# Kernel tuning notes

Measured on AMD Instinct MI355X. Metric: run time of the kernel, lower is better.

The kernel has to match this reference:

```python
import jax, jax.numpy as jnp
import numpy as np

B, S, D, H, FFN = 4, 1024, 1024, 16, 4096
DH = D // H
EPS = 1e-5
NEG = -1e20


def _layer_norm(t, g, b):
    m = jnp.mean(t, axis=-1, keepdims=True)
    v = jnp.mean((t - m) ** 2, axis=-1, keepdims=True)
    return (t - m) / jnp.sqrt(v + EPS) * g + b


def setup_inputs() -> dict:
    key = jax.random.key(0)
    ks = jax.random.split(key, 16)
    std_attn = np.sqrt(2.0 / (D + D)).astype(np.float32)  # xavier normal
    lim1 = np.sqrt(6.0 / (D + FFN)).astype(np.float32)    # xavier uniform
    inp = {
        'tensor': jax.random.normal(ks[0], (B, S, D), jnp.float32),
        'mask': jnp.ones((B, S), jnp.int32),
        'wq': jax.random.normal(ks[1], (D, D), jnp.float32) * std_attn,
        'bq': jnp.zeros((D,), jnp.float32),
        'wk': jax.random.normal(ks[2], (D, D), jnp.float32) * std_attn,
        'bk': jnp.zeros((D,), jnp.float32),
        'wv': jax.random.normal(ks[3], (D, D), jnp.float32) * std_attn,
        'bv': jnp.zeros((D,), jnp.float32),
        'wo': jax.random.normal(ks[4], (D, D), jnp.float32) * std_attn,
        'bo': jnp.zeros((D,), jnp.float32),
        'ln1_g': jnp.ones((D,), jnp.float32),
        'ln1_b': jnp.zeros((D,), jnp.float32),
        'w1': jax.random.uniform(ks[5], (FFN, D), jnp.float32, -lim1, lim1),
        'b1': jnp.zeros((FFN,), jnp.float32),
        'w2': jax.random.uniform(ks[6], (D, FFN), jnp.float32, -lim1, lim1),
        'b2': jnp.zeros((D,), jnp.float32),
        'ln2_g': jnp.ones((D,), jnp.float32),
        'ln2_b': jnp.zeros((D,), jnp.float32),
    }
    return inp


def reference(tensor, mask, wq, bq, wk, bk, wv, bv, wo, bo,
              ln1_g, ln1_b, w1, b1, w2, b2, ln2_g, ln2_b):
    x = tensor
    scale = jnp.sqrt(jnp.float32(DH))
    # QKV projections -> [B, S, H, DH]
    q = (x @ wq.T + bq).reshape(B, S, H, DH)
    k = (x @ wk.T + bk).reshape(B, S, H, DH)
    v = (x @ wv.T + bv).reshape(B, S, H, DH)
    # scores [B, H, Sq, Sk]
    scores = jnp.einsum('bqhd,bkhd->bhqk', q / scale, k)
    blocked = (mask == 0)[:, None, None, :]  # True -> block
    scores = jnp.where(blocked, NEG, scores)
    attn = jax.nn.softmax(scores.astype(jnp.float32), axis=-1).astype(x.dtype)
    ctx = jnp.einsum('bhqk,bkhd->bqhd', attn, v).reshape(B, S, D)
    attn_out = ctx @ wo.T + bo
    # post-LN (variant='aiayn')
    t = _layer_norm(x + attn_out, ln1_g, ln1_b)
    ffn = jax.nn.relu(t @ w1.T + b1) @ w2.T + b2
    t = _layer_norm(t + ffn, ln2_g, ln2_b)
    t = t * mask[:, :, None].astype(t.dtype)
    return t
```

## Files before the change

### kernel.cpp

```cpp
#include <hip/hip_runtime.h>

typedef __bf16 bf16x8 __attribute__((ext_vector_type(8)));
typedef __bf16 bf16x4 __attribute__((ext_vector_type(4)));
typedef float f32x4 __attribute__((ext_vector_type(4)));
typedef float f32x16 __attribute__((ext_vector_type(16)));

#define BB 4
#define SS 1024
#define DD 1024
#define HH 16
#define DHH 64
#define FFN 4096

__device__ __forceinline__ void gload_lds16(const void* g, void* lds) {
  __builtin_amdgcn_global_load_lds(
      (const __attribute__((address_space(1))) unsigned int*)g,
      (__attribute__((address_space(3))) unsigned int*)lds, 16, 0, 0);
}

__global__ __launch_bounds__(256) void cvt_all_kernel(
    const float* __restrict__ x, const float* __restrict__ wq, const float* __restrict__ wk,
    const float* __restrict__ wv, const float* __restrict__ wo, const float* __restrict__ w1,
    const float* __restrict__ w2, __bf16* __restrict__ xb, __bf16* __restrict__ wqkvb,
    __bf16* __restrict__ wob, __bf16* __restrict__ w1b, __bf16* __restrict__ w2b)
{
  int i = blockIdx.x * 256 + threadIdx.x;
  const float* src; __bf16* dst; int off;
  if (i < 524288)       { src = x;  dst = xb;              off = i; }
  else if (i < 655360)  { src = wq; dst = wqkvb;           off = i - 524288; }
  else if (i < 786432)  { src = wk; dst = wqkvb + 1048576; off = i - 655360; }
  else if (i < 917504)  { src = wv; dst = wqkvb + 2097152; off = i - 786432; }
  else if (i < 1048576) { src = wo; dst = wob;             off = i - 917504; }
  else if (i < 1572864) { src = w1; dst = w1b;             off = i - 1048576; }
  else                  { src = w2; dst = w2b;             off = i - 1572864; }
  float4 a = *(const float4*)(src + off * 8);
  float4 b = *(const float4*)(src + off * 8 + 4);
  bf16x8 v;
  v[0] = (__bf16)a.x; v[1] = (__bf16)a.y; v[2] = (__bf16)a.z; v[3] = (__bf16)a.w;
  v[4] = (__bf16)b.x; v[5] = (__bf16)b.y; v[6] = (__bf16)b.z; v[7] = (__bf16)b.w;
  *(bf16x8*)(dst + off * 8) = v;
}

template<int MODE>
__global__ __launch_bounds__(512, 2) void gemm_8ph(
    const __bf16* __restrict__ Ag, const __bf16* __restrict__ Bg,
    const float* __restrict__ bias, void* __restrict__ outp,
    int M, int N, int K)
{
  __shared__ __bf16 LdsEl[65536];
  char* L = (char*)LdsEl;
  const int tid = threadIdx.x, wid = tid >> 6, lane = tid & 63;
  const int wm = wid >> 2, wn = wid & 3, bh = wn >> 1;
  const int lr = lane & 15, lg = lane >> 4;
  const int l8 = lane >> 3, l7 = lane & 7;

  const int gx = gridDim.x, nwg = gx * gridDim.y;
  const int wg = blockIdx.y * gx + blockIdx.x;
  const int swz = (wg & 7) * (nwg >> 3) + (wg >> 3);
  const int bm = (swz / gx) * 256, bn = (swz % gx) * 256;

  const int rowA0 = wn * 32;
  const int rowB0 = (wn & 1) * 64 + wm * 32;
  const size_t gAr = (size_t)(bm + wm * 128 + rowA0);
  const size_t gBr = (size_t)(bn + bh * 128 + rowB0);

  const __bf16* srcA[4]; const __bf16* srcB[4];
#pragma unroll
  for (int c = 0; c < 4; ++c) {
    int rwA = rowA0 + c * 8 + l8;
    int scA = (l7 * 16) ^ (((rwA >> 2) & 1) << 5);
    srcA[c] = Ag + (gAr + c * 8 + l8) * K + (scA >> 1);
    int rwB = rowB0 + c * 8 + l8;
    int scB = (l7 * 16) ^ (((rwB >> 2) & 1) << 5);
    srcB[c] = Bg + (gBr + c * 8 + l8) * K + (scB >> 1);
  }
  char* dA = L + wm * 16384 + rowA0 * 128;
  char* dB = L + 65536 + bh * 16384 + rowB0 * 128;

#define STGA4(TAU, KT) do { const int kt_ = (KT) * 64; \
    gload_lds16(srcA[0] + kt_, dA + (TAU) * 32768);          \
    gload_lds16(srcA[1] + kt_, dA + (TAU) * 32768 + 1024);   \
    gload_lds16(srcA[2] + kt_, dA + (TAU) * 32768 + 2048);   \
    gload_lds16(srcA[3] + kt_, dA + (TAU) * 32768 + 3072); } while (0)
#define STGB4(TAU, KT) do { const int kt_ = (KT) * 64; \
    gload_lds16(srcB[0] + kt_, dB + (TAU) * 32768);          \
    gload_lds16(srcB[1] + kt_, dB + (TAU) * 32768 + 1024);   \
    gload_lds16(srcB[2] + kt_, dB + (TAU) * 32768 + 2048);   \
    gload_lds16(srcB[3] + kt_, dB + (TAU) * 32768 + 3072); } while (0)

  f32x4 acc[8][4] = {};

  STGA4(0, 0); STGB4(0, 0); STGA4(1, 1); STGB4(1, 1);
  asm volatile("s_waitcnt vmcnt(0)" ::: "memory");
  __builtin_amdgcn_s_barrier();

#define PHASE(TAU, KS, IH, STGCODE, WAITCODE) do { \
    bf16x8 af[4]; \
    _Pragma("unroll") for (int i = 0; i < 4; ++i) { \
      int row = (IH) * 64 + i * 16 + lr; \
      int cb = ((KS) * 64 + lg * 16) ^ (((row >> 2) & 1) << 5); \
      af[i] = *(const bf16x8*)(L + ((TAU) * 2 + wm) * 16384 + row * 128 + cb); } \
    if ((IH) == 0) { \
      _Pragma("unroll") for (int j = 0; j < 4; ++j) { \
        int row = (wn & 1) * 64 + j * 16 + lr; \
        int cb = ((KS) * 64 + lg * 16) ^ (((row >> 2) & 1) << 5); \
        bfr[j] = *(const bf16x8*)(L + 65536 + ((TAU) * 2 + bh) * 16384 + row * 128 + cb); } } \
    STGCODE; \
    __builtin_amdgcn_s_barrier(); \
    __builtin_amdgcn_s_setprio(1); \
    _Pragma("unroll") for (int i = 0; i < 4; ++i) \
    _Pragma("unroll") for (int j = 0; j < 4; ++j) \
      acc[(IH) * 4 + i][j] = __builtin_amdgcn_mfma_f32_16x16x32_bf16(af[i], bfr[j], acc[(IH) * 4 + i][j], 0, 0, 0); \
    __builtin_amdgcn_s_setprio(0); \
    WAITCODE; \
    __builtin_amdgcn_s_barrier(); \
  } while (0)

  const int NT = K >> 7;
#pragma unroll 1
  for (int t = 0; t < NT; ++t) {
    const bool s1 = (t > 0);
    const bool s0 = (t + 1 < NT);
    bf16x8 bfr[4];
    PHASE(0, 0, 0, { if (s1) STGA4(1, 2 * t + 1); }, {});
    PHASE(0, 0, 1, { if (s1) STGB4(1, 2 * t + 1); }, {});
    PHASE(0, 1, 0, {}, {});
    PHASE(0, 1, 1, {}, { asm volatile("s_waitcnt vmcnt(0)" ::: "memory"); });
    PHASE(1, 0, 0, { if (s0) STGA4(0, 2 * t + 2); }, {});
    PHASE(1, 0, 1, { if (s0) STGB4(0, 2 * t + 2); }, {});
    PHASE(1, 1, 0, {}, {});
    PHASE(1, 1, 1, {}, { asm volatile("s_waitcnt vmcnt(0)" ::: "memory"); });
  }
#undef PHASE
#undef STGA4
#undef STGB4

#pragma unroll
  for (int ih = 0; ih < 2; ++ih)
#pragma unroll
    for (int i = 0; i < 4; ++i)
#pragma unroll
      for (int j = 0; j < 4; ++j)
#pragma unroll
        for (int r = 0; r < 4; ++r) {
          int row = bm + wm * 128 + ih * 64 + i * 16 + lg * 4 + r;
          int col = bn + wn * 64 + j * 16 + lr;
          float v = acc[ih * 4 + i][j][r];
          if constexpr (MODE == 3) {
            float t2 = v + bias[col];
            ((__bf16*)outp)[(size_t)row * N + col] = (__bf16)fmaxf(t2, 0.f);
          }
        }
}

template<int MODE>
__global__ __launch_bounds__(256, 2) void gemm_bt(
    const __bf16* __restrict__ A, const __bf16* __restrict__ Bw,
    const float* __restrict__ bias, const float* __restrict__ bias1, const float* __restrict__ bias2,
    const float* __restrict__ res, void* __restrict__ outp, void* __restrict__ out1,
    int M, int N, int K, int kLen, float scale)
{
  __shared__ __bf16 As[2][128 * 32];
  __shared__ __bf16 Bs[2][128 * 32];
  const int tid = threadIdx.x;
  const int wid = tid >> 6;
  const int lane = tid & 63;
  const int lr = lane & 15;
  const int lg = lane >> 4;

  const int gx = gridDim.x;
  const int nwg = gx * gridDim.y;
  const int wg = blockIdx.y * gx + blockIdx.x;
  const int swz = (wg & 7) * (nwg >> 3) + (wg >> 3);
  const int bm = (swz / gx) * 128;
  const int bn = (swz % gx) * 128;

  const int wm = (wid >> 1) * 64;
  const int wn = (wid & 1) * 64;

  int kBeg = 0, nk = K >> 5;
  if constexpr (MODE == 5) { kBeg = blockIdx.z * kLen; nk = kLen >> 5; }

  const int off = tid * 16;
  const int srow = off >> 6;
  const int scol = (off & 63) >> 1;
  const __bf16* gA0 = A + (size_t)(bm + srow) * K + kBeg + scol;
  const __bf16* gA1 = A + (size_t)(bm + 64 + srow) * K + kBeg + scol;
  const __bf16* gB0 = Bw + (size_t)(bn + srow) * K + kBeg + scol;
  const __bf16* gB1 = Bw + (size_t)(bn + 64 + srow) * K + kBeg + scol;
  char* lA = (char*)&As[0][0] + wid * 1024;
  char* lB = (char*)&Bs[0][0] + wid * 1024;

  f32x4 acc[4][4] = {};

#define STAGE(buf, kk) do { \
    gload_lds16(gA0 + (kk), lA + (buf) * 8192); \
    gload_lds16(gA1 + (kk), lA + (buf) * 8192 + 4096); \
    gload_lds16(gB0 + (kk), lB + (buf) * 8192); \
    gload_lds16(gB1 + (kk), lB + (buf) * 8192 + 4096); \
  } while (0)

  STAGE(0, 0);
  __syncthreads();
  for (int t = 0; t < nk; ++t) {
    const int cur = t & 1;
    if (t + 1 < nk) STAGE(cur ^ 1, (t + 1) << 5);
    bf16x8 af[4], bv[4];
#pragma unroll
    for (int i = 0; i < 4; ++i)
      af[i] = *(const bf16x8*)&As[cur][(wm + i * 16 + lr) * 32 + lg * 8];
#pragma unroll
    for (int i = 0; i < 4; ++i)
      bv[i] = *(const bf16x8*)&Bs[cur][(wn + i * 16 + lr) * 32 + lg * 8];
#pragma unroll
    for (int i = 0; i < 4; ++i)
#pragma unroll
      for (int j = 0; j < 4; ++j)
        acc[i][j] = __builtin_amdgcn_mfma_f32_16x16x32_bf16(af[i], bv[j], acc[i][j], 0, 0, 0);
    __syncthreads();
  }
#undef STAGE

#pragma unroll
  for (int i = 0; i < 4; ++i) {
#pragma unroll
    for (int j = 0; j < 4; ++j) {
#pragma unroll
      for (int r = 0; r < 4; ++r) {
        int row = bm + wm + i * 16 + lg * 4 + r;
        int col = bn + wn + j * 16 + lr;
        float v = acc[i][j][r];
        if constexpr (MODE == 2) {
          size_t idx = (size_t)row * N + col;
          ((float*)outp)[idx] = v + bias[col] + res[idx];
        } else if constexpr (MODE == 3) {
          float t2 = v + bias[col];
          ((__bf16*)outp)[(size_t)row * N + col] = (__bf16)fmaxf(t2, 0.f);
        } else if constexpr (MODE == 4) {
          int region = col >> 10;
          int col_ = col & 1023;
          int b_ = row >> 10, s_ = row & 1023;
          int h_ = col_ >> 6, d_ = col_ & 63;
          if (region == 0) {
            float v2 = (v + bias[col_]) * scale;
            ((__bf16*)outp)[(((size_t)(b_ * HH + h_) * SS) + s_) * DHH + d_] = (__bf16)v2;
          } else if (region == 1) {
            float v2 = v + bias1[col_];
            ((__bf16*)out1)[(((size_t)(b_ * HH + h_) * SS) + s_) * DHH + d_] = (__bf16)v2;
          } else {
            float v2 = v + bias2[col_];
            ((__bf16*)res)[(((size_t)(b_ * HH + h_) * DHH) + d_) * SS + s_] = (__bf16)v2;
          }
        } else {
          float* dst = blockIdx.z ? (float*)out1 : (float*)outp;
          dst[(size_t)row * N + col] = v;
        }
      }
    }
  }
}

__global__ __launch_bounds__(256, 2) void attn_kernel(
    const __bf16* __restrict__ q, const __bf16* __restrict__ k,
    const __bf16* __restrict__ vt, const int* __restrict__ mask,
    __bf16* __restrict__ ctx)
{
  const int nwg = gridDim.x;
  const int wg = blockIdx.x;
  const int swzb = (wg & 7) * (nwg >> 3) + (wg >> 3);
  const int bh = swzb >> 3;
  const int qb = (swzb & 7) << 7;
  const int b = bh >> 4;

  const int tid = threadIdx.x, wid = tid >> 6, lane = tid & 63;
  const int ln = lane & 31, hi = lane >> 5;

  __shared__ __bf16 Kt[2][64 * 64];
  __shared__ __bf16 Vt[2][64 * 64];
  __shared__ __bf16 Pt[4][32 * 64];
  __shared__ float mmulLds[SS];

  {
    const int* mrow = mask + b * SS;
    int c = tid * 4;
    float4 mm;
    mm.x = (float)(mrow[c + 0] != 0);
    mm.y = (float)(mrow[c + 1] != 0);
    mm.z = (float)(mrow[c + 2] != 0);
    mm.w = (float)(mrow[c + 3] != 0);
    ((float4*)mmulLds)[tid] = mm;
  }

  const __bf16* qh = q + (size_t)bh * SS * DHH;
  const __bf16* kh = k + (size_t)bh * SS * DHH;
  const __bf16* vh = vt + (size_t)bh * DHH * SS;

  const int qw = qb + wid * 32;
  bf16x8 qf[4];
#pragma unroll
  for (int s = 0; s < 4; ++s)
    qf[s] = *(const bf16x8*)&qh[(size_t)(qw + ln) * DHH + s * 16 + hi * 8];

  const int srow = tid >> 3;
  const int ps = tid & 7;
  const int sw0 = (srow ^ (srow >> 3)) & 7;
  const int r1 = srow + 32;
  const int sw1 = (r1 ^ (r1 >> 3)) & 7;
  const __bf16* kS0 = kh + (size_t)srow * DHH + ((ps ^ sw0) * 8);
  const __bf16* kS1 = kh + (size_t)r1 * DHH + ((ps ^ sw1) * 8);
  const __bf16* vS0 = vh + (size_t)srow * SS + ((ps ^ sw0) * 8);
  const __bf16* vS1 = vh + (size_t)r1 * SS + ((ps ^ sw1) * 8);

#define ASTAGE(bufi, kb_) do { \
    gload_lds16(kS0 + (size_t)(kb_) * DHH, (char*)&Kt[bufi][0] + wid * 1024); \
    gload_lds16(kS1 + (size_t)(kb_) * DHH, (char*)&Kt[bufi][0] + wid * 1024 + 4096); \
    gload_lds16(vS0 + (kb_), (char*)&Vt[bufi][0] + wid * 1024); \
    gload_lds16(vS1 + (kb_), (char*)&Vt[bufi][0] + wid * 1024 + 4096); \
  } while (0)

  char* Pw = (char*)&Pt[wid][0];
  const int swA = (ln ^ (ln >> 3)) & 7;
  const int swB = swA ^ 4;

  f32x16 o0 = {}, o1 = {};
  float l[16];
#pragma unroll
  for (int r = 0; r < 16; ++r) l[r] = 0.f;

  ASTAGE(0, 0);
  __syncthreads();

#pragma unroll 1
  for (int t = 0; t < SS / 64; ++t) {
    const int cur = t & 1;
    const int kb = t * 64;
    if (t + 1 < SS / 64) ASTAGE(cur ^ 1, kb + 64);

    const char* Kc = (const char*)&Kt[cur][0];
    const char* Vc = (const char*)&Vt[cur][0];

    f32x16 sc0 = {}, sc1 = {};
#pragma unroll
    for (int s = 0; s < 4; ++s) {
      bf16x8 kb0 = *(const bf16x8*)(Kc + ln * 128 + (((s * 2 + hi) ^ swA) << 4));
      bf16x8 kb1 = *(const bf16x8*)(Kc + (32 + ln) * 128 + (((s * 2 + hi) ^ swB) << 4));
      sc0 = __builtin_amdgcn_mfma_f32_32x32x16_bf16(qf[s], kb0, sc0, 0, 0, 0);
      sc1 = __builtin_amdgcn_mfma_f32_32x32x16_bf16(qf[s], kb1, sc1, 0, 0, 0);
    }

    float mm0 = mmulLds[kb + ln];
    float mm1 = mmulLds[kb + 32 + ln];
#pragma unroll
    for (int r = 0; r < 16; ++r) {
      float p0 = exp2f(sc0[r] - 23.0831207f) * mm0;
      float p1 = exp2f(sc1[r] - 23.0831207f) * mm1;
      l[r] += p0 + p1;
      int qrow = (r & 3) + 8 * (r >> 2) + 4 * hi;
      int swq = (qrow ^ (qrow >> 3)) & 7;
      *(__bf16*)(Pw + qrow * 128 + ((((ln >> 3) + 0) ^ swq) << 4) + (ln & 7) * 2) = (__bf16)p0;
      *(__bf16*)(Pw + qrow * 128 + ((((ln >> 3) + 4) ^ swq) << 4) + (ln & 7) * 2) = (__bf16)p1;
    }

#pragma unroll
    for (int ks = 0; ks < 4; ++ks) {
      bf16x8 pa = *(const bf16x8*)(Pw + ln * 128 + (((ks * 2 + hi) ^ swA) << 4));
      bf16x8 vb0 = *(const bf16x8*)(Vc + ln * 128 + (((ks * 2 + hi) ^ swA) << 4));
      bf16x8 vb1 = *(const bf16x8*)(Vc + (32 + ln) * 128 + (((ks * 2 + hi) ^ swB) << 4));
      o0 = __builtin_amdgcn_mfma_f32_32x32x16_bf16(pa, vb0, o0, 0, 0, 0);
      o1 = __builtin_amdgcn_mfma_f32_32x32x16_bf16(pa, vb1, o1, 0, 0, 0);
    }
    __syncthreads();
  }
#undef ASTAGE

#pragma unroll
  for (int r = 0; r < 16; ++r) {
#pragma unroll
    for (int off = 1; off < 32; off <<= 1) l[r] += __shfl_xor(l[r], off);
  }

#pragma unroll
  for (int r = 0; r < 16; ++r) {
    float inv = l[r] > 0.f ? 1.f / l[r] : 0.f;
    int qrow = (r & 3) + 8 * (r >> 2) + 4 * hi;
    size_t base = ((size_t)b * SS + qw + qrow) * DD + (size_t)(bh & 15) * DHH;
    ctx[base + ln] = (__bf16)(o0[r] * inv);
    ctx[base + 32 + ln] = (__bf16)(o1[r] * inv);
  }
}

__global__ __launch_bounds__(256) void ln_kernel(
    const float* __restrict__ in, const float* __restrict__ g, const float* __restrict__ b,
    float* __restrict__ out32, __bf16* __restrict__ out16)
{
  int row = blockIdx.x;
  int tid = threadIdx.x;
  int wid = tid >> 6, lane = tid & 63;
  float4 v = ((const float4*)(in + (size_t)row * DD))[tid];
  float s = v.x + v.y + v.z + v.w;
  float sq = v.x * v.x + v.y * v.y + v.z * v.z + v.w * v.w;
#pragma unroll
  for (int o = 1; o < 64; o <<= 1) { s += __shfl_xor(s, o); sq += __shfl_xor(sq, o); }
  __shared__ float red[8];
  if (lane == 0) { red[wid] = s; red[4 + wid] = sq; }
  __syncthreads();
  s = red[0] + red[1] + red[2] + red[3];
  sq = red[4] + red[5] + red[6] + red[7];
  float mean = s * (1.f / DD);
  float var = sq * (1.f / DD) - mean * mean;
  float rstd = rsqrtf(var + 1e-5f);
  float4 gg = ((const float4*)g)[tid];
  float4 bb = ((const float4*)b)[tid];
  float4 o;
  o.x = (v.x - mean) * rstd * gg.x + bb.x;
  o.y = (v.y - mean) * rstd * gg.y + bb.y;
  o.z = (v.z - mean) * rstd * gg.z + bb.z;
  o.w = (v.w - mean) * rstd * gg.w + bb.w;
  if (out32) ((float4*)(out32 + (size_t)row * DD))[tid] = o;
  if (out16) {
    bf16x4 w;
    w[0] = (__bf16)o.x; w[1] = (__bf16)o.y; w[2] = (__bf16)o.z; w[3] = (__bf16)o.w;
    *(bf16x4*)(out16 + (size_t)row * DD + tid * 4) = w;
  }
}

__global__ __launch_bounds__(256) void ln2_fused_kernel(
    const float* __restrict__ p0, const float* __restrict__ p1, const float* __restrict__ bias,
    const float* __restrict__ res, const float* __restrict__ g, const float* __restrict__ b,
    const int* __restrict__ mask, float* __restrict__ out)
{
  int row = blockIdx.x;
  int tid = threadIdx.x;
  int wid = tid >> 6, lane = tid & 63;
  size_t base = (size_t)row * DD;
  float4 a0 = ((const float4*)(p0 + base))[tid];
  float4 a1 = ((const float4*)(p1 + base))[tid];
  float4 rr = ((const float4*)(res + base))[tid];
  float4 bs = ((const float4*)bias)[tid];
  float4 v;
  v.x = a0.x + a1.x + rr.x + bs.x;
  v.y = a0.y + a1.y + rr.y + bs.y;
  v.z = a0.z + a1.z + rr.z + bs.z;
  v.w = a0.w + a1.w + rr.w + bs.w;
  float s = v.x + v.y + v.z + v.w;
  float sq = v.x * v.x + v.y * v.y + v.z * v.z + v.w * v.w;
#pragma unroll
  for (int o = 1; o < 64; o <<= 1) { s += __shfl_xor(s, o); sq += __shfl_xor(sq, o); }
  __shared__ float red[8];
  if (lane == 0) { red[wid] = s; red[4 + wid] = sq; }
  __syncthreads();
  s = red[0] + red[1] + red[2] + red[3];
  sq = red[4] + red[5] + red[6] + red[7];
  float mean = s * (1.f / DD);
  float var = sq * (1.f / DD) - mean * mean;
  float rstd = rsqrtf(var + 1e-5f);
  float4 gg = ((const float4*)g)[tid];
  float4 bb = ((const float4*)b)[tid];
  float mk = (float)mask[row];
  float4 o;
  o.x = ((v.x - mean) * rstd * gg.x + bb.x) * mk;
  o.y = ((v.y - mean) * rstd * gg.y + bb.y) * mk;
  o.z = ((v.z - mean) * rstd * gg.z + bb.z) * mk;
  o.w = ((v.w - mean) * rstd * gg.w + bb.w) * mk;
  ((float4*)(out + base))[tid] = o;
}

extern "C" void kernel_launch(void* const* d_in, const int* in_sizes, int n_in,
                              void* d_out, int out_size, void* d_ws, size_t ws_size,
                              hipStream_t stream) {
  const float* x    = (const float*)d_in[0];
  const int*  mask  = (const int*)d_in[1];
  const float* wq   = (const float*)d_in[2];
  const float* bq   = (const float*)d_in[3];
  const float* wk   = (const float*)d_in[4];
  const float* bk   = (const float*)d_in[5];
  const float* wv   = (const float*)d_in[6];
  const float* bv   = (const float*)d_in[7];
  const float* wo   = (const float*)d_in[8];
  const float* bo   = (const float*)d_in[9];
  const float* ln1g = (const float*)d_in[10];
  const float* ln1b = (const float*)d_in[11];
  const float* w1   = (const float*)d_in[12];
  const float* b1   = (const float*)d_in[13];
  const float* w2   = (const float*)d_in[14];
  const float* b2   = (const float*)d_in[15];
  const float* ln2g = (const float*)d_in[16];
  const float* ln2b = (const float*)d_in[17];
  float* out = (float*)d_out;
  char* ws = (char*)d_ws;

  __bf16* xb    = (__bf16*)(ws + 0);
  __bf16* wqkvb = (__bf16*)(ws + 8388608);
  __bf16* wob   = (__bf16*)(ws + 14680064);
  __bf16* w1b   = (__bf16*)(ws + 16777216);
  __bf16* w2b   = (__bf16*)(ws + 25165824);
  __bf16* qbuf  = (__bf16*)(ws + 33554432);
  __bf16* kbuf  = (__bf16*)(ws + 41943040);
  __bf16* vtbf  = (__bf16*)(ws + 50331648);
  __bf16* ctxb  = (__bf16*)(ws + 58720256);
  __bf16* hb    = (__bf16*)(ws + 33554432);
  float*  r1    = (float*)(ws + 67108864);
  float*  t32   = (float*)(ws + 83886080);
  __bf16* tb    = (__bf16*)(ws + 100663296);
  float*  p0    = r1;
  float*  p1    = (float*)(ws + 0);

  const int MSD = BB * SS;

  cvt_all_kernel<<<8192, 256, 0, stream>>>(x, wq, wk, wv, wo, w1, w2, xb, wqkvb, wob, w1b, w2b);

  gemm_bt<4><<<dim3(24, 32), 256, 0, stream>>>(xb, wqkvb, bq, bk, bv, (const float*)vtbf,
                                               qbuf, kbuf, MSD, 3072, DD, 0, 0.18033688f);

  attn_kernel<<<BB * HH * (SS / 128), 256, 0, stream>>>(qbuf, kbuf, vtbf, mask, ctxb);

  gemm_bt<2><<<dim3(8, 32), 256, 0, stream>>>(ctxb, wob, bo, nullptr, nullptr, x,
                                              r1, nullptr, MSD, DD, DD, 0, 1.0f);
  ln_kernel<<<MSD, 256, 0, stream>>>(r1, ln1g, ln1b, t32, tb);

  gemm_8ph<3><<<dim3(16, 16), 512, 0, stream>>>(tb, w1b, b1, hb, MSD, FFN, DD);

  gemm_bt<3><<<dim3(32, 32), 256, 0, stream>>>(tb, w1b, b1, nullptr, nullptr, nullptr,
                                               hb, nullptr, MSD, FFN, DD, 0, 1.0f);
  gemm_bt<5><<<dim3(8, 32, 2), 256, 0, stream>>>(hb, w2b, nullptr, nullptr, nullptr, nullptr,
                                                 p0, p1, MSD, DD, FFN, 2048, 1.0f);
  ln2_fused_kernel<<<MSD, 256, 0, stream>>>(p0, p1, b2, t32, ln2g, ln2b, mask, out);
}
```

Baseline: 272.5 us.

## Move QKV GEMM to 256-tile 8-phase kernel and add 4-stage FFN1 GEMM

Result: slower. 284.6 us (+4.5%).

```diff
diff --git a/kernel.cpp b/kernel.cpp
--- a/kernel.cpp
+++ b/kernel.cpp
@@ -44,8 +44,10 @@
 template<int MODE>
 __global__ __launch_bounds__(512, 2) void gemm_8ph(
     const __bf16* __restrict__ Ag, const __bf16* __restrict__ Bg,
-    const float* __restrict__ bias, void* __restrict__ outp,
-    int M, int N, int K)
+    const float* __restrict__ bias, const float* __restrict__ bias1,
+    const float* __restrict__ bias2, const float* __restrict__ res,
+    void* __restrict__ outp, void* __restrict__ out1,
+    int M, int N, int K, float scale)
 {
   __shared__ __bf16 LdsEl[65536];
   char* L = (char*)LdsEl;
@@ -149,6 +151,126 @@
           if constexpr (MODE == 3) {
             float t2 = v + bias[col];
             ((__bf16*)outp)[(size_t)row * N + col] = (__bf16)fmaxf(t2, 0.f);
+          } else if constexpr (MODE == 4) {
+            int region = col >> 10;
+            int col_ = col & 1023;
+            int b_ = row >> 10, s_ = row & 1023;
+            int h_ = col_ >> 6, d_ = col_ & 63;
+            if (region == 0) {
+              float v2 = (v + bias[col_]) * scale;
+              ((__bf16*)outp)[(((size_t)(b_ * HH + h_) * SS) + s_) * DHH + d_] = (__bf16)v2;
+            } else if (region == 1) {
+              float v2 = v + bias1[col_];
+              ((__bf16*)out1)[(((size_t)(b_ * HH + h_) * SS) + s_) * DHH + d_] = (__bf16)v2;
+            } else {
+              float v2 = v + bias2[col_];
+              ((__bf16*)res)[(((size_t)(b_ * HH + h_) * DHH) + d_) * SS + s_] = (__bf16)v2;
+            }
+          }
+        }
+}
+
+template<int MODE>
+__global__ __launch_bounds__(512, 2) void gemm_r4(
+    const __bf16* __restrict__ Ag, const __bf16* __restrict__ Bg,
+    const float* __restrict__ bias, void* __restrict__ outp,
+    int M, int N, int K)
+{
+  __shared__ __bf16 LdsEl[65536];
+  char* L = (char*)LdsEl;
+  const int tid = threadIdx.x, wid = tid >> 6, lane = tid & 63;
+  const int wm = wid >> 2, wn = wid & 3, bh = wn >> 1;
+  const int lr = lane & 15, lg = lane >> 4;
+
+  const int gx = gridDim.x, nwg = gx * gridDim.y;
+  const int wg = blockIdx.y * gx + blockIdx.x;
+  const int swz = (wg & 7) * (nwg >> 3) + (wg >> 3);
+  const int bm = (swz / gx) * 256, bn = (swz % gx) * 256;
+
+  const int rowA0 = wn * 32;
+  const int rowB0 = (wn & 1) * 64 + wm * 32;
+  const __bf16* srcA[2]; const __bf16* srcB[2];
+#pragma unroll
+  for (int c = 0; c < 2; ++c) {
+    int ra = rowA0 + c * 16 + (lane >> 2);
+    srcA[c] = Ag + (size_t)(bm + wm * 128 + ra) * K + (((lane & 3) ^ (ra & 3)) << 3);
+    int rb = rowB0 + c * 16 + (lane >> 2);
+    srcB[c] = Bg + (size_t)(bn + bh * 128 + rb) * K + (((lane & 3) ^ (rb & 3)) << 3);
+  }
+  char* dA = L + wm * 8192 + rowA0 * 64;
+  char* dB = L + 65536 + bh * 8192 + rowB0 * 64;
+
+#define STGA(TAU, KT) do { \
+    gload_lds16(srcA[0] + (KT) * 32, dA + (TAU) * 16384); \
+    gload_lds16(srcA[1] + (KT) * 32, dA + (TAU) * 16384 + 1024); } while (0)
+#define STGB(TAU, KT) do { \
+    gload_lds16(srcB[0] + (KT) * 32, dB + (TAU) * 16384); \
+    gload_lds16(srcB[1] + (KT) * 32, dB + (TAU) * 16384 + 1024); } while (0)
+
+  f32x4 acc[8][4] = {};
+  const int NK = K >> 5;
+
+  STGA(0, 0); STGB(0, 0); STGA(1, 1); STGB(1, 1); STGA(2, 2); STGB(2, 2);
+
+  const int sA = (lg ^ (lr & 3)) << 4;
+
+#pragma unroll 1
+  for (int k = 0; k < NK; ++k) {
+    const int tau = k & 3;
+    const int kn = (k + 3 < NK) ? (k + 3) : (NK - 1);
+    const int tn = (k + 3) & 3;
+    asm volatile("s_waitcnt vmcnt(8)" ::: "memory");
+    __builtin_amdgcn_s_barrier();
+    __builtin_amdgcn_sched_barrier(0);
+    const char* Ac = L + (tau * 2 + wm) * 8192;
+    const char* Bc = L + 65536 + (tau * 2 + bh) * 8192;
+    bf16x8 bfr[4], af0[4], af1[4];
+#pragma unroll
+    for (int j = 0; j < 4; ++j)
+      bfr[j] = *(const bf16x8*)(Bc + ((wn & 1) * 64 + j * 16 + lr) * 64 + sA);
+#pragma unroll
+    for (int i = 0; i < 4; ++i)
+      af0[i] = *(const bf16x8*)(Ac + (i * 16 + lr) * 64 + sA);
+    STGA(tn, kn);
+    __builtin_amdgcn_s_barrier();
+    __builtin_amdgcn_s_setprio(1);
+#pragma unroll
+    for (int i = 0; i < 4; ++i)
+#pragma unroll
+      for (int j = 0; j < 4; ++j)
+        acc[i][j] = __builtin_amdgcn_mfma_f32_16x16x32_bf16(af0[i], bfr[j], acc[i][j], 0, 0, 0);
+    __builtin_amdgcn_s_setprio(0);
+#pragma unroll
+    for (int i = 0; i < 4; ++i)
+      af1[i] = *(const bf16x8*)(Ac + (64 + i * 16 + lr) * 64 + sA);
+    STGB(tn, kn);
+    __builtin_amdgcn_s_barrier();
+    __builtin_amdgcn_s_setprio(1);
+#pragma unroll
+    for (int i = 0; i < 4; ++i)
+#pragma unroll
+      for (int j = 0; j < 4; ++j)
+        acc[4 + i][j] = __builtin_amdgcn_mfma_f32_16x16x32_bf16(af1[i], bfr[j], acc[4 + i][j], 0, 0, 0);
+    __builtin_amdgcn_s_setprio(0);
+  }
+#undef STGA
+#undef STGB
+  asm volatile("s_waitcnt vmcnt(0)" ::: "memory");
+
+#pragma unroll
+  for (int ih = 0; ih < 2; ++ih)
+#pragma unroll
+    for (int i = 0; i < 4; ++i)
+#pragma unroll
+      for (int j = 0; j < 4; ++j)
+#pragma unroll
+        for (int r = 0; r < 4; ++r) {
+          int row = bm + wm * 128 + ih * 64 + i * 16 + lg * 4 + r;
+          int col = bn + wn * 64 + j * 16 + lr;
+          float v = acc[ih * 4 + i][j][r];
+          if constexpr (MODE == 3) {
+            float t2 = v + bias[col];
+            ((__bf16*)outp)[(size_t)row * N + col] = (__bf16)fmaxf(t2, 0.f);
           }
         }
 }
@@ -156,9 +278,9 @@
 template<int MODE>
 __global__ __launch_bounds__(256, 2) void gemm_bt(
     const __bf16* __restrict__ A, const __bf16* __restrict__ Bw,
-    const float* __restrict__ bias, const float* __restrict__ bias1, const float* __restrict__ bias2,
-    const float* __restrict__ res, void* __restrict__ outp, void* __restrict__ out1,
-    int M, int N, int K, int kLen, float scale)
+    const float* __restrict__ bias, const float* __restrict__ res,
+    void* __restrict__ outp, void* __restrict__ out1,
+    int M, int N, int K, int kLen)
 {
   __shared__ __bf16 As[2][128 * 32];
   __shared__ __bf16 Bs[2][128 * 32];
@@ -233,24 +355,6 @@
         if constexpr (MODE == 2) {
           size_t idx = (size_t)row * N + col;
           ((float*)outp)[idx] = v + bias[col] + res[idx];
-        } else if constexpr (MODE == 3) {
-          float t2 = v + bias[col];
-          ((__bf16*)outp)[(size_t)row * N + col] = (__bf16)fmaxf(t2, 0.f);
-        } else if constexpr (MODE == 4) {
-          int region = col >> 10;
-          int col_ = col & 1023;
-          int b_ = row >> 10, s_ = row & 1023;
-          int h_ = col_ >> 6, d_ = col_ & 63;
-          if (region == 0) {
-            float v2 = (v + bias[col_]) * scale;
-            ((__bf16*)outp)[(((size_t)(b_ * HH + h_) * SS) + s_) * DHH + d_] = (__bf16)v2;
-          } else if (region == 1) {
-            float v2 = v + bias1[col_];
-            ((__bf16*)out1)[(((size_t)(b_ * HH + h_) * SS) + s_) * DHH + d_] = (__bf16)v2;
-          } else {
-            float v2 = v + bias2[col_];
-            ((__bf16*)res)[(((size_t)(b_ * HH + h_) * DHH) + d_) * SS + s_] = (__bf16)v2;
-          }
         } else {
           float* dst = blockIdx.z ? (float*)out1 : (float*)outp;
           dst[(size_t)row * N + col] = v;
@@ -509,20 +613,20 @@
 
   cvt_all_kernel<<<8192, 256, 0, stream>>>(x, wq, wk, wv, wo, w1, w2, xb, wqkvb, wob, w1b, w2b);
 
-  gemm_bt<4><<<dim3(24, 32), 256, 0, stream>>>(xb, wqkvb, bq, bk, bv, (const float*)vtbf,
-                                               qbuf, kbuf, MSD, 3072, DD, 0, 0.18033688f);
+  gemm_8ph<4><<<dim3(12, 16), 512, 0, stream>>>(
+      xb, wqkvb, bq, bk, bv, (const float*)vtbf, qbuf, kbuf, MSD, 3072, DD, 0.18033688f);
 
   attn_kernel<<<BB * HH * (SS / 128), 256, 0, stream>>>(qbuf, kbuf, vtbf, mask, ctxb);
 
-  gemm_bt<2><<<dim3(8, 32), 256, 0, stream>>>(ctxb, wob, bo, nullptr, nullptr, x,
-                                              r1, nullptr, MSD, DD, DD, 0, 1.0f);
+  gemm_bt<2><<<dim3(8, 32), 256, 0, stream>>>(ctxb, wob, bo, x, r1, nullptr, MSD, DD, DD, 0);
   ln_kernel<<<MSD, 256, 0, stream>>>(r1, ln1g, ln1b, t32, tb);
 
-  gemm_8ph<3><<<dim3(16, 16), 512, 0, stream>>>(tb, w1b, b1, hb, MSD, FFN, DD);
-
-  gemm_bt<3><<<dim3(32, 32), 256, 0, stream>>>(tb, w1b, b1, nullptr, nullptr, nullptr,
-                                               hb, nullptr, MSD, FFN, DD, 0, 1.0f);
-  gemm_bt<5><<<dim3(8, 32, 2), 256, 0, stream>>>(hb, w2b, nullptr, nullptr, nullptr, nullptr,
-                                                 p0, p1, MSD, DD, FFN, 2048, 1.0f);
+  gemm_r4<3><<<dim3(16, 16), 512, 0, stream>>>(tb, w1b, b1, hb, MSD, FFN, DD);
+
+  gemm_8ph<3><<<dim3(16, 16), 512, 0, stream>>>(
+      tb, w1b, b1, nullptr, nullptr, nullptr, hb, nullptr, MSD, FFN, DD, 1.0f);
+
+  gemm_bt<5><<<dim3(8, 32, 2), 256, 0, stream>>>(hb, w2b, nullptr, nullptr, p0, p1,
+                                                 MSD, DD, FFN, 2048);
   ln2_fused_kernel<<<MSD, 256, 0, stream>>>(p0, p1, b2, t32, ln2g, ln2b, mask, out);
 }
```
